# Optimization experiments

Hardware: AMD Instinct MI355X
Metric: run time of the kernel (lower is better)

Reference implementation:

```python
import jax, jax.numpy as jnp
import numpy as np
import math

B, N, D, H, O = 2, 1024, 256, 4, 8
DT, STEPS = 0.1, 5


def setup_inputs() -> dict:
    key = jax.random.key(0)
    ks = jax.random.split(key, 8)
    inv_d = 1.0 / math.sqrt(D)
    inv_ho = 1.0 / math.sqrt(H * O)
    return {
        "x": jax.random.normal(ks[0], (B, N, D), jnp.float32),
        "Wq": jax.random.normal(ks[1], (D, D), jnp.float32) * inv_d,
        "Wk": jax.random.normal(ks[2], (D, D), jnp.float32) * inv_d,
        "Wp": jax.random.normal(ks[3], (H * O, D), jnp.float32) * inv_d,
        "bp": jnp.zeros((H * O,), jnp.float32),
        "Wo": jax.random.normal(ks[4], (D, H * O), jnp.float32) * inv_ho,
        "bo": jnp.zeros((D,), jnp.float32),
        "omega": jax.random.normal(ks[5], (H, O), jnp.float32) * 0.1,
        "coupling_scale": jnp.asarray(1.0, jnp.float32),
    }


def reference(x, Wq, Wk, Wp, bp, Wo, bo, omega, coupling_scale):
    dk = D // H
    # attention coupling J_ij = softmax(q_i.k_j / sqrt(d_k))  -> (B,H,N,N)
    q = (x @ Wq.T).reshape(B, N, H, dk).transpose(0, 2, 1, 3)
    k = (x @ Wk.T).reshape(B, N, H, dk).transpose(0, 2, 1, 3)
    J = jax.nn.softmax(jnp.einsum('bhid,bhjd->bhij', q, k) / math.sqrt(dk), axis=-1)
    # initial phases (B,H,N,O)
    phases = (x @ Wp.T + bp).reshape(B, N, H, O).transpose(0, 2, 1, 3)
    om = omega[None, :, None, :]  # (1,H,1,O)

    def step(ph, _):
        # sum_j J_ij sin(phi_j - phi_i) = cos(phi_i)*(J@sin phi) - sin(phi_i)*(J@cos phi)
        s, c = jnp.sin(ph), jnp.cos(ph)
        coupling = c * jnp.einsum('bhij,bhjo->bhio', J, s) - s * jnp.einsum('bhij,bhjo->bhio', J, c)
        new = ph + DT * (om + coupling_scale * coupling)
        new = jnp.remainder(new + jnp.pi, 2 * jnp.pi) - jnp.pi
        return new, None

    phases, _ = jax.lax.scan(step, phases, None, length=STEPS)
    sig = jnp.cos(phases).transpose(0, 2, 1, 3).reshape(B, N, H * O)
    return sig @ Wo.T + bo
```

## Files before the change

### kernel.cpp

```cpp
#include <hip/hip_runtime.h>
#include <hip/hip_bf16.h>
#include <math.h>


#define NB 1024
#define NH 4
#define DD 256
#define NO 8
#define PI_F      3.14159265358979323846f
#define TWO_PI_F  6.28318530717958647692f
#define INV_2PI_F 0.15915494309189533577f

typedef __attribute__((ext_vector_type(8))) short bf16x8;
typedef __attribute__((ext_vector_type(4))) float f32x4;

__device__ __forceinline__ float b2f_u(unsigned short s) {
    union { unsigned u; float f; } x; x.u = ((unsigned)s) << 16; return x.f;
}
__device__ __forceinline__ unsigned short f2b(float f) {
    union { float f; unsigned u; } v; v.f = f;
    unsigned r = v.u + 0x7FFFu + ((v.u >> 16) & 1u);
    return (unsigned short)(r >> 16);
}
template<bool F32>
__device__ __forceinline__ float load1(const void* p, int i) {
    if (F32) return ((const float*)p)[i];
    else     return b2f_u(((const unsigned short*)p)[i]);
}
template<bool F32>
__device__ __forceinline__ void load8(const void* p, int i, float* f) {
    if (F32) {
        const float* fp = (const float*)p + i;
        float4 a = *(const float4*)(fp);
        float4 b = *(const float4*)(fp + 4);
        f[0]=a.x; f[1]=a.y; f[2]=a.z; f[3]=a.w;
        f[4]=b.x; f[5]=b.y; f[6]=b.z; f[7]=b.w;
    } else {
        uint4 u = *(const uint4*)((const unsigned short*)p + i);
        f[0] = b2f_u(u.x & 0xFFFFu); f[1] = b2f_u(u.x >> 16);
        f[2] = b2f_u(u.y & 0xFFFFu); f[3] = b2f_u(u.y >> 16);
        f[4] = b2f_u(u.z & 0xFFFFu); f[5] = b2f_u(u.z >> 16);
        f[6] = b2f_u(u.w & 0xFFFFu); f[7] = b2f_u(u.w >> 16);
    }
}
__device__ __forceinline__ float read_cs_bf16(const void* p) {
    float vb = b2f_u(*(const unsigned short*)p);
    bool ok = isfinite(vb) && fabsf(vb) > 1e-30f && fabsf(vb) < 1e30f;
    if (ok) return vb;
    return *(const float*)p;
}

__global__ void k_detect(const unsigned short* __restrict__ x, int* __restrict__ flag)
{
    int l = threadIdx.x & 63;
    float v0 = b2f_u(x[2 * l]);
    float v1 = b2f_u(x[2 * (l + 64)]);
    float a0 = fabsf(v0), a1 = fabsf(v1);
    unsigned long long b0 = __ballot(!(a0 >= 1e-10f && a0 <= 100.0f));
    unsigned long long b1 = __ballot(!(a1 >= 1e-10f && a1 <= 100.0f));
    if (l == 0) *flag = ((__popcll(b0) + __popcll(b1)) > 16) ? 1 : 0;
}

__global__ __launch_bounds__(256) void k_prep(
    const int* __restrict__ flag,
    const void* __restrict__ x, const void* __restrict__ Wq,
    const void* __restrict__ Wk, const void* __restrict__ Wp,
    unsigned short* __restrict__ xb, unsigned short* __restrict__ Wall)
{
    const int idx = blockIdx.x * 256 + threadIdx.x;
    const int f32 = *flag;
    if (idx < 524288) {
        float v = f32 ? ((const float*)x)[idx] : b2f_u(((const unsigned short*)x)[idx]);
        xb[idx] = f2b(v);
    } else {
        int w = idx - 524288;
        int row = w >> 8, col = w & 255;
        float v = 0.f;
        if (row < 256)      v = f32 ? ((const float*)Wq)[row*256+col] : b2f_u(((const unsigned short*)Wq)[row*256+col]);
        else if (row < 512) v = f32 ? ((const float*)Wk)[(row-256)*256+col] : b2f_u(((const unsigned short*)Wk)[(row-256)*256+col]);
        else if (row < 544) v = f32 ? ((const float*)Wp)[(row-512)*256+col] : b2f_u(((const unsigned short*)Wp)[(row-512)*256+col]);
        Wall[w] = f2b(v);
    }
}

__global__ __launch_bounds__(256) void k_projm(
    const int* __restrict__ flag,
    const unsigned short* __restrict__ xb, const unsigned short* __restrict__ Wall,
    const void* __restrict__ bp,
    unsigned short* __restrict__ Qb, unsigned short* __restrict__ Kb,
    float* __restrict__ PH)
{
    __shared__ uint4 Xsh[64 * 32];
    __shared__ uint4 Wsh[64 * 32];
    const int tid = threadIdx.x;
    const int gx = blockIdx.x;
    const int ftile = gx % 9, itile = gx / 9;
    const int i0 = itile * 64, f0 = ftile * 64;
    const int wave = tid >> 6, lane = tid & 63;
    const int n = lane & 15, quad = lane >> 4;

    #pragma unroll
    for (int g = 0; g < 8; g++) {
        int fidx = g * 256 + tid;
        int row = fidx >> 5, q = fidx & 31;
        int sw = (q & 24) | ((q ^ row) & 7);
        Xsh[row * 32 + sw] = *(const uint4*)(xb + (size_t)(i0 + row) * 256 + q * 8);
        Wsh[row * 32 + sw] = *(const uint4*)(Wall + (size_t)(f0 + row) * 256 + q * 8);
    }
    __syncthreads();

    f32x4 acc[4];
    #pragma unroll
    for (int s = 0; s < 4; s++) acc[s] = (f32x4){0.f, 0.f, 0.f, 0.f};
    const int xrow = wave * 16 + n;
    #pragma unroll
    for (int s = 0; s < 8; s++) {
        int qc = s * 4 + quad;
        bf16x8 b = ((const bf16x8*)Xsh)[xrow * 32 + ((qc & 24) | ((qc ^ xrow) & 7))];
        #pragma unroll
        for (int sub = 0; sub < 4; sub++) {
            int wr = sub * 16 + n;
            bf16x8 a = ((const bf16x8*)Wsh)[wr * 32 + ((qc & 24) | ((qc ^ wr) & 7))];
            acc[sub] = __builtin_amdgcn_mfma_f32_16x16x32_bf16(a, b, acc[sub], 0, 0, 0);
        }
    }

    const int ig = i0 + wave * 16 + n;
    const int bb = ig >> 10, nr = ig & 1023;
    if (ftile < 4) {
        #pragma unroll
        for (int sub = 0; sub < 4; sub++) {
            int dd = sub * 16 + quad * 4;
            ushort4 v = make_ushort4(f2b(acc[sub][0] * 0.125f), f2b(acc[sub][1] * 0.125f),
                                     f2b(acc[sub][2] * 0.125f), f2b(acc[sub][3] * 0.125f));
            *(ushort4*)(Qb + ((size_t)((bb * NH + ftile) * NB + nr)) * 64 + dd) = v;
        }
    } else if (ftile < 8) {
        int h = ftile - 4;
        #pragma unroll
        for (int sub = 0; sub < 4; sub++) {
            int dd = sub * 16 + quad * 4;
            ushort4 v = make_ushort4(f2b(acc[sub][0]), f2b(acc[sub][1]),
                                     f2b(acc[sub][2]), f2b(acc[sub][3]));
            *(ushort4*)(Kb + ((size_t)((bb * NH + h) * NB + nr)) * 64 + dd) = v;
        }
    } else {
        const int f32 = *flag;
        #pragma unroll
        for (int sub = 0; sub < 2; sub++) {
            #pragma unroll
            for (int r = 0; r < 4; r++) {
                int fp = sub * 16 + quad * 4 + r;
                int h2 = fp >> 3, o = fp & 7;
                float bpv = f32 ? ((const float*)bp)[fp] : b2f_u(((const unsigned short*)bp)[fp]);
                PH[((size_t)(bb * NH + h2)) * 8192 + o * 1024 + nr] = acc[sub][r] + bpv;
            }
        }
    }
}

__global__ __launch_bounds__(256) void k_scores(
    const unsigned short* __restrict__ Qb, const unsigned short* __restrict__ Kb,
    unsigned short* __restrict__ U, float* __restrict__ R)
{
    __shared__ uint4 Ksh[512 * 8];
    __shared__ float redS[2][2][16];
    const int tid = threadIdx.x;
    const int bh  = blockIdx.x >> 5;
    const int wave = tid >> 6, lane = tid & 63;
    const int n = lane & 15, quad = lane >> 4;
    const int iw = wave >> 1, jw = wave & 1;
    const int i0 = (blockIdx.x & 31) * 32 + iw * 16;

    const unsigned short* qrow = Qb + ((size_t)(bh * NB) + i0 + n) * 64;
    bf16x8 bq0 = *(const bf16x8*)(qrow + quad * 8);
    bf16x8 bq1 = *(const bf16x8*)(qrow + 32 + quad * 8);

    float s = 0.f;
    unsigned short* urow = U + ((size_t)(bh * NB) + i0 + n) * NB;
    #pragma unroll 1
    for (int half = 0; half < 2; half++) {
        __syncthreads();
        const unsigned short* ksrc = Kb + ((size_t)(bh * NB) + half * 512) * 64;
        #pragma unroll
        for (int g = 0; g < 16; g++) {
            int fidx = g * 256 + tid;
            int rl = fidx >> 3, q = fidx & 7;
            Ksh[rl * 8 + (q ^ (rl & 7))] = *(const uint4*)(ksrc + fidx * 8);
        }
        __syncthreads();
        for (int t = 0; t < 16; t++) {
            int jt = jw * 16 + t;
            int rl = jt * 16 + n;
            bf16x8 a0 = ((const bf16x8*)Ksh)[rl * 8 + (quad ^ (n & 7))];
            bf16x8 a1 = ((const bf16x8*)Ksh)[rl * 8 + ((4 + quad) ^ (n & 7))];
            f32x4 acc = {0.f, 0.f, 0.f, 0.f};
            acc = __builtin_amdgcn_mfma_f32_16x16x32_bf16(a0, bq0, acc, 0, 0, 0);
            acc = __builtin_amdgcn_mfma_f32_16x16x32_bf16(a1, bq1, acc, 0, 0, 0);
            float u0 = __expf(acc[0]);
            float u1 = __expf(acc[1]);
            float u2 = __expf(acc[2]);
            float u3 = __expf(acc[3]);
            s += (u0 + u1) + (u2 + u3);
            ushort4 uv = make_ushort4(f2b(u0), f2b(u1), f2b(u2), f2b(u3));
            *(ushort4*)(urow + half * 512 + jt * 16 + quad * 4) = uv;
        }
    }
    s += __shfl_xor(s, 16);
    s += __shfl_xor(s, 32);
    if (lane < 16) redS[iw][jw][lane] = s;
    __syncthreads();
    if (jw == 0 && lane < 16)
        R[bh * NB + i0 + lane] = 1.0f / (redS[iw][0][lane] + redS[iw][1][lane]);
}

__global__ __launch_bounds__(256) void k_step(
    const int* __restrict__ flag,
    const unsigned short* __restrict__ U, const float* __restrict__ R,
    const float* __restrict__ PHin, float* __restrict__ PHout,
    const void* __restrict__ omega, const void* __restrict__ csp)
{
    __shared__ uint4 sc4[16 * 128];
    __shared__ f32x4 red[4][64];
    const int tid  = threadIdx.x;
    const int bh   = blockIdx.x >> 6;
    const int i0   = (blockIdx.x & 63) * 16;
    const int wave = tid >> 6, lane = tid & 63;
    const int n    = lane & 15, quad = lane >> 4;
    const float* phs = PHin + (size_t)bh * 8192;

    #pragma unroll
    for (int g = 0; g < 8; g++) {
        float4 pv = *(const float4*)(phs + g * 1024 + tid * 4);
        float s0, c0, s1, c1, s2, c2, s3, c3;
        __sincosf(pv.x, &s0, &c0); __sincosf(pv.y, &s1, &c1);
        __sincosf(pv.z, &s2, &c2); __sincosf(pv.w, &s3, &c3);
        ushort4 sv = make_ushort4(f2b(s0), f2b(s1), f2b(s2), f2b(s3));
        ushort4 cv = make_ushort4(f2b(c0), f2b(c1), f2b(c2), f2b(c3));
        int ci = (tid >> 1) ^ (g & 7);
        char* base = (char*)sc4;
        *(ushort4*)(base + (((g     ) * 128 + ci) << 4) + ((tid & 1) << 3)) = sv;
        *(ushort4*)(base + (((g +  8) * 128 + ci) << 4) + ((tid & 1) << 3)) = cv;
    }
    __syncthreads();

    const unsigned short* urow = U + ((size_t)(bh * NB) + i0 + n) * NB;
    f32x4 acc = {0.f, 0.f, 0.f, 0.f};
    #pragma unroll
    for (int t = 0; t < 8; t++) {
        int it = wave * 8 + t;
        bf16x8 a = *(const bf16x8*)(urow + it * 32 + quad * 8);
        bf16x8 b = ((const bf16x8*)sc4)[n * 128 + ((it * 4 + quad) ^ (n & 7))];
        acc = __builtin_amdgcn_mfma_f32_16x16x32_bf16(a, b, acc, 0, 0, 0);
    }
    red[wave][lane] = acc;
    __syncthreads();

    if (wave == 0) {
        f32x4 a0 = red[0][lane], a1 = red[1][lane];
        f32x4 a2 = red[2][lane], a3 = red[3][lane];
        #pragma unroll
        for (int v = 0; v < 4; v++) acc[v] = (a0[v] + a1[v]) + (a2[v] + a3[v]);

        float C0 = __shfl_xor(acc[0], 8);
        float C1 = __shfl_xor(acc[1], 8);
        float C2 = __shfl_xor(acc[2], 8);
        float C3 = __shfl_xor(acc[3], 8);

        if (n < 8) {
            const int o = n, h = bh & 3;
            const int f32 = *flag;
            const float cs = f32 ? *(const float*)csp : read_cs_bf16(csp);
            const float om = f32 ? ((const float*)omega)[h * NO + o]
                                 : b2f_u(((const unsigned short*)omega)[h * NO + o]);
            float4 Rv = *(const float4*)(R + bh * NB + i0 + quad * 4);
            float4 pv = *(const float4*)(phs + o * 1024 + i0 + quad * 4);
            float S[4] = {acc[0], acc[1], acc[2], acc[3]};
            float C[4] = {C0, C1, C2, C3};
            float Rr[4] = {Rv.x, Rv.y, Rv.z, Rv.w};
            float P[4]  = {pv.x, pv.y, pv.z, pv.w};
            float outp[4];
            #pragma unroll
            for (int r = 0; r < 4; r++) {
                float si, ci;
                __sincosf(P[r], &si, &ci);
                float coup = (ci * S[r] - si * C[r]) * Rr[r];
                float v = P[r] + 0.1f * (om + cs * coup);
                float t = v + PI_F;
                t -= floorf(t * INV_2PI_F) * TWO_PI_F;
                outp[r] = t - PI_F;
            }
            float4 ov = {outp[0], outp[1], outp[2], outp[3]};
            *(float4*)(PHout + (size_t)bh * 8192 + o * 1024 + i0 + quad * 4) = ov;
        }
    }
}

template<bool F32>
__device__ void out_impl(
    const float* __restrict__ PH,
    const void* __restrict__ Wo, const void* __restrict__ bo,
    void* __restrict__ out)
{
    __shared__ float sig[32];
    const int tid = threadIdx.x;
    const int b = blockIdx.x >> 10, n = blockIdx.x & 1023;
    if (tid < 32) {
        int h = tid >> 3, o = tid & 7;
        sig[tid] = __cosf(PH[(size_t)(b * NH + h) * 8192 + o * 1024 + n]);
    }
    __syncthreads();
    float acc = load1<F32>(bo, tid);
    #pragma unroll
    for (int d0 = 0; d0 < 32; d0 += 8) {
        float w[8];
        load8<F32>(Wo, tid * 32 + d0, w);
        #pragma unroll
        for (int t = 0; t < 8; t++) acc += sig[d0 + t] * w[t];
    }
    size_t oi = (size_t)blockIdx.x * DD + tid;
    if (F32) ((float*)out)[oi] = acc;
    else     ((__hip_bfloat16*)out)[oi] = __float2bfloat16(acc);
}

__global__ __launch_bounds__(256) void k_out(
    const int* __restrict__ flag,
    const float* PH, const void* Wo, const void* bo, void* out)
{
    if (*flag) out_impl<true >(PH, Wo, bo, out);
    else       out_impl<false>(PH, Wo, bo, out);
}

extern "C" void kernel_launch(void* const* d_in, const int* in_sizes, int n_in,
                              void* d_out, int out_size, void* d_ws, size_t ws_size,
                              hipStream_t stream)
{
    const void* x   = d_in[0];
    const void* Wq  = d_in[1];
    const void* Wk  = d_in[2];
    const void* Wp  = d_in[3];
    const void* bp  = d_in[4];
    const void* Wo  = d_in[5];
    const void* bo  = d_in[6];
    const void* om  = d_in[7];
    const void* cs  = d_in[8];

    char* w = (char*)d_ws;
    int*            flag = (int*)w;
    unsigned short* Qb   = (unsigned short*)(w + 256);
    unsigned short* Kb   = (unsigned short*)(w + 256 + (1u << 20));
    float*          R    = (float*)(w + 256 + (2u << 20));
    float*          PH0  = (float*)(w + 256 + (2u << 20) + (64u << 10));
    float*          PH1  = (float*)(w + 256 + (2u << 20) + (320u << 10));
    unsigned short* U    = (unsigned short*)(w + 256 + (2u << 20) + (576u << 10));
    unsigned short* xb   = (unsigned short*)(w + 256 + (2u << 20) + (576u << 10) + (16u << 20));
    unsigned short* Wall = (unsigned short*)(w + 256 + (2u << 20) + (576u << 10) + (17u << 20));

    k_detect<<<1,    64,  0, stream>>>((const unsigned short*)x, flag);
    k_prep  <<<2624, 256, 0, stream>>>(flag, x, Wq, Wk, Wp, xb, Wall);
    k_projm <<<288,  256, 0, stream>>>(flag, xb, Wall, bp, Qb, Kb, PH0);
    k_scores<<<256,  256, 0, stream>>>(Qb, Kb, U, R);
    k_step<<<512, 256, 0, stream>>>(flag, U, R, PH0, PH1, om, cs);
    k_step<<<512, 256, 0, stream>>>(flag, U, R, PH1, PH0, om, cs);
    k_step<<<512, 256, 0, stream>>>(flag, U, R, PH0, PH1, om, cs);
    k_step<<<512, 256, 0, stream>>>(flag, U, R, PH1, PH0, om, cs);
    k_step<<<512, 256, 0, stream>>>(flag, U, R, PH0, PH1, om, cs);
    k_out<<<2048, 256, 0, stream>>>(flag, PH1, Wo, bo, d_out);
}
```

Measured before the change: 137.4 us.

## Fuse dtype detection and bf16 conversion into projection; precompute sin/cos tables

Removes the separate detect and prep kernels: each kernel now detects the input dtype inline, and the projection kernel converts fp32 inputs to bf16 while loading them into shared memory. The phase kernels now write bf16 sin/cos tables of the new phases, so the next step loads them directly instead of recomputing sincos for all 8192 phases per block. The output kernel reads cos from that table. This cuts two launches and redundant transcendental work. In exchange it adds scattered 2-byte writes of sin/cos and repeats the detection work in every block.

```diff
diff --git a/kernel.cpp b/kernel.cpp
--- a/kernel.cpp
+++ b/kernel.cpp
@@ -23,15 +23,22 @@
     return (unsigned short)(r >> 16);
 }
 template<bool F32>
-__device__ __forceinline__ float load1(const void* p, int i) {
-    if (F32) return ((const float*)p)[i];
-    else     return b2f_u(((const unsigned short*)p)[i]);
-}
-template<bool F32>
-__device__ __forceinline__ void load8(const void* p, int i, float* f) {
-    if (F32) {
+__device__ __forceinline__ uint4 load_pack8(const void* p, size_t off) {
+    if (!F32) return *(const uint4*)((const unsigned short*)p + off);
+    const float* fp = (const float*)p + off;
+    float4 a = *(const float4*)fp;
+    float4 b = *(const float4*)(fp + 4);
+    uint4 r;
+    r.x = (unsigned)f2b(a.x) | ((unsigned)f2b(a.y) << 16);
+    r.y = (unsigned)f2b(a.z) | ((unsigned)f2b(a.w) << 16);
+    r.z = (unsigned)f2b(b.x) | ((unsigned)f2b(b.y) << 16);
+    r.w = (unsigned)f2b(b.z) | ((unsigned)f2b(b.w) << 16);
+    return r;
+}
+__device__ __forceinline__ void load8_rt(int f32, const void* p, int i, float* f) {
+    if (f32) {
         const float* fp = (const float*)p + i;
-        float4 a = *(const float4*)(fp);
+        float4 a = *(const float4*)fp;
         float4 b = *(const float4*)(fp + 4);
         f[0]=a.x; f[1]=a.y; f[2]=a.z; f[3]=a.w;
         f[4]=b.x; f[5]=b.y; f[6]=b.z; f[7]=b.w;
@@ -49,52 +56,27 @@
     if (ok) return vb;
     return *(const float*)p;
 }
-
-__global__ void k_detect(const unsigned short* __restrict__ x, int* __restrict__ flag)
-{
+__device__ __forceinline__ int detect_inline(const unsigned short* x) {
     int l = threadIdx.x & 63;
-    float v0 = b2f_u(x[2 * l]);
-    float v1 = b2f_u(x[2 * (l + 64)]);
-    float a0 = fabsf(v0), a1 = fabsf(v1);
+    float a0 = fabsf(b2f_u(x[2 * l]));
+    float a1 = fabsf(b2f_u(x[2 * (l + 64)]));
     unsigned long long b0 = __ballot(!(a0 >= 1e-10f && a0 <= 100.0f));
     unsigned long long b1 = __ballot(!(a1 >= 1e-10f && a1 <= 100.0f));
-    if (l == 0) *flag = ((__popcll(b0) + __popcll(b1)) > 16) ? 1 : 0;
-}
-
-__global__ __launch_bounds__(256) void k_prep(
-    const int* __restrict__ flag,
+    return (__popcll(b0) + __popcll(b1)) > 16;
+}
+
+template<bool F32>
+__device__ void projm_impl(
     const void* __restrict__ x, const void* __restrict__ Wq,
     const void* __restrict__ Wk, const void* __restrict__ Wp,
-    unsigned short* __restrict__ xb, unsigned short* __restrict__ Wall)
-{
-    const int idx = blockIdx.x * 256 + threadIdx.x;
-    const int f32 = *flag;
-    if (idx < 524288) {
-        float v = f32 ? ((const float*)x)[idx] : b2f_u(((const unsigned short*)x)[idx]);
-        xb[idx] = f2b(v);
-    } else {
-        int w = idx - 524288;
-        int row = w >> 8, col = w & 255;
-        float v = 0.f;
-        if (row < 256)      v = f32 ? ((const float*)Wq)[row*256+col] : b2f_u(((const unsigned short*)Wq)[row*256+col]);
-        else if (row < 512) v = f32 ? ((const float*)Wk)[(row-256)*256+col] : b2f_u(((const unsigned short*)Wk)[(row-256)*256+col]);
-        else if (row < 544) v = f32 ? ((const float*)Wp)[(row-512)*256+col] : b2f_u(((const unsigned short*)Wp)[(row-512)*256+col]);
-        Wall[w] = f2b(v);
-    }
-}
-
-__global__ __launch_bounds__(256) void k_projm(
-    const int* __restrict__ flag,
-    const unsigned short* __restrict__ xb, const unsigned short* __restrict__ Wall,
     const void* __restrict__ bp,
     unsigned short* __restrict__ Qb, unsigned short* __restrict__ Kb,
-    float* __restrict__ PH)
+    float* __restrict__ PH, unsigned short* __restrict__ SC)
 {
     __shared__ uint4 Xsh[64 * 32];
     __shared__ uint4 Wsh[64 * 32];
     const int tid = threadIdx.x;
-    const int gx = blockIdx.x;
-    const int ftile = gx % 9, itile = gx / 9;
+    const int ftile = blockIdx.x % 9, itile = blockIdx.x / 9;
     const int i0 = itile * 64, f0 = ftile * 64;
     const int wave = tid >> 6, lane = tid & 63;
     const int n = lane & 15, quad = lane >> 4;
@@ -104,8 +86,13 @@
         int fidx = g * 256 + tid;
         int row = fidx >> 5, q = fidx & 31;
         int sw = (q & 24) | ((q ^ row) & 7);
-        Xsh[row * 32 + sw] = *(const uint4*)(xb + (size_t)(i0 + row) * 256 + q * 8);
-        Wsh[row * 32 + sw] = *(const uint4*)(Wall + (size_t)(f0 + row) * 256 + q * 8);
+        Xsh[row * 32 + sw] = load_pack8<F32>(x, (size_t)(i0 + row) * 256 + q * 8);
+        int wr = f0 + row;
+        uint4 wv = make_uint4(0, 0, 0, 0);
+        if (wr < 256)      wv = load_pack8<F32>(Wq, (size_t)wr * 256 + q * 8);
+        else if (wr < 512) wv = load_pack8<F32>(Wk, (size_t)(wr - 256) * 256 + q * 8);
+        else if (wr < 544) wv = load_pack8<F32>(Wp, (size_t)(wr - 512) * 256 + q * 8);
+        Wsh[row * 32 + sw] = wv;
     }
     __syncthreads();
 
@@ -145,18 +132,33 @@
             *(ushort4*)(Kb + ((size_t)((bb * NH + h) * NB + nr)) * 64 + dd) = v;
         }
     } else {
-        const int f32 = *flag;
         #pragma unroll
         for (int sub = 0; sub < 2; sub++) {
             #pragma unroll
             for (int r = 0; r < 4; r++) {
                 int fp = sub * 16 + quad * 4 + r;
                 int h2 = fp >> 3, o = fp & 7;
-                float bpv = f32 ? ((const float*)bp)[fp] : b2f_u(((const unsigned short*)bp)[fp]);
-                PH[((size_t)(bb * NH + h2)) * 8192 + o * 1024 + nr] = acc[sub][r] + bpv;
+                float bpv = F32 ? ((const float*)bp)[fp]
+                                : b2f_u(((const unsigned short*)bp)[fp]);
+                float v = acc[sub][r] + bpv;
+                int bh = bb * NH + h2;
+                PH[(size_t)bh * 8192 + o * 1024 + nr] = v;
+                float sv, cv;
+                __sincosf(v, &sv, &cv);
+                SC[(size_t)(bh * 16 + o) * 1024 + nr]     = f2b(sv);
+                SC[(size_t)(bh * 16 + 8 + o) * 1024 + nr] = f2b(cv);
             }
         }
     }
+}
+
+__global__ __launch_bounds__(256) void k_projm(
+    const unsigned short* x, const void* Wq, const void* Wk, const void* Wp,
+    const void* bp, unsigned short* Qb, unsigned short* Kb, float* PH,
+    unsigned short* SC)
+{
+    if (detect_inline(x)) projm_impl<true >(x, Wq, Wk, Wp, bp, Qb, Kb, PH, SC);
+    else                  projm_impl<false>(x, Wq, Wk, Wp, bp, Qb, Kb, PH, SC);
 }
 
 __global__ __launch_bounds__(256) void k_scores(
@@ -202,8 +204,8 @@
             float u2 = __expf(acc[2]);
             float u3 = __expf(acc[3]);
             s += (u0 + u1) + (u2 + u3);
-            ushort4 uv = make_ushort4(f2b(u0), f2b(u1), f2b(u2), f2b(u3));
-            *(ushort4*)(urow + half * 512 + jt * 16 + quad * 4) = uv;
+            *(ushort4*)(urow + half * 512 + jt * 16 + quad * 4)
+                = make_ushort4(f2b(u0), f2b(u1), f2b(u2), f2b(u3));
         }
     }
     s += __shfl_xor(s, 16);
@@ -215,9 +217,10 @@
 }
 
 __global__ __launch_bounds__(256) void k_step(
-    const int* __restrict__ flag,
+    const unsigned short* __restrict__ xraw,
     const unsigned short* __restrict__ U, const float* __restrict__ R,
     const float* __restrict__ PHin, float* __restrict__ PHout,
+    const unsigned short* __restrict__ SCin, unsigned short* __restrict__ SCout,
     const void* __restrict__ omega, const void* __restrict__ csp)
 {
     __shared__ uint4 sc4[16 * 128];
@@ -227,20 +230,15 @@
     const int i0   = (blockIdx.x & 63) * 16;
     const int wave = tid >> 6, lane = tid & 63;
     const int n    = lane & 15, quad = lane >> 4;
+    const int f32  = detect_inline(xraw);
     const float* phs = PHin + (size_t)bh * 8192;
 
     #pragma unroll
     for (int g = 0; g < 8; g++) {
-        float4 pv = *(const float4*)(phs + g * 1024 + tid * 4);
-        float s0, c0, s1, c1, s2, c2, s3, c3;
-        __sincosf(pv.x, &s0, &c0); __sincosf(pv.y, &s1, &c1);
-        __sincosf(pv.z, &s2, &c2); __sincosf(pv.w, &s3, &c3);
-        ushort4 sv = make_ushort4(f2b(s0), f2b(s1), f2b(s2), f2b(s3));
-        ushort4 cv = make_ushort4(f2b(c0), f2b(c1), f2b(c2), f2b(c3));
-        int ci = (tid >> 1) ^ (g & 7);
-        char* base = (char*)sc4;
-        *(ushort4*)(base + (((g     ) * 128 + ci) << 4) + ((tid & 1) << 3)) = sv;
-        *(ushort4*)(base + (((g +  8) * 128 + ci) << 4) + ((tid & 1) << 3)) = cv;
+        int fidx = g * 256 + tid;
+        int row = fidx >> 7, col = fidx & 127;
+        sc4[row * 128 + (col ^ (row & 7))]
+            = *(const uint4*)(SCin + (size_t)(bh * 16 + row) * 1024 + col * 8);
     }
     __syncthreads();
 
@@ -269,7 +267,6 @@
 
         if (n < 8) {
             const int o = n, h = bh & 3;
-            const int f32 = *flag;
             const float cs = f32 ? *(const float*)csp : read_cs_bf16(csp);
             const float om = f32 ? ((const float*)omega)[h * NO + o]
                                  : b2f_u(((const unsigned short*)omega)[h * NO + o]);
@@ -279,63 +276,64 @@
             float C[4] = {C0, C1, C2, C3};
             float Rr[4] = {Rv.x, Rv.y, Rv.z, Rv.w};
             float P[4]  = {pv.x, pv.y, pv.z, pv.w};
-            float outp[4];
+            float op[4];
             #pragma unroll
             for (int r = 0; r < 4; r++) {
                 float si, ci;
                 __sincosf(P[r], &si, &ci);
                 float coup = (ci * S[r] - si * C[r]) * Rr[r];
                 float v = P[r] + 0.1f * (om + cs * coup);
-                float t = v + PI_F;
-                t -= floorf(t * INV_2PI_F) * TWO_PI_F;
-                outp[r] = t - PI_F;
+                float t2 = v + PI_F;
+                t2 -= floorf(t2 * INV_2PI_F) * TWO_PI_F;
+                op[r] = t2 - PI_F;
             }
-            float4 ov = {outp[0], outp[1], outp[2], outp[3]};
-            *(float4*)(PHout + (size_t)bh * 8192 + o * 1024 + i0 + quad * 4) = ov;
-        }
-    }
-}
-
-template<bool F32>
-__device__ void out_impl(
-    const float* __restrict__ PH,
+            *(float4*)(PHout + (size_t)bh * 8192 + o * 1024 + i0 + quad * 4)
+                = make_float4(op[0], op[1], op[2], op[3]);
+            #pragma unroll
+            for (int r = 0; r < 4; r++) {
+                float sn, cn;
+                __sincosf(op[r], &sn, &cn);
+                int i = i0 + quad * 4 + r;
+                SCout[(size_t)(bh * 16 + o) * 1024 + i]     = f2b(sn);
+                SCout[(size_t)(bh * 16 + 8 + o) * 1024 + i] = f2b(cn);
+            }
+        }
+    }
+}
+
+__global__ __launch_bounds__(256) void k_out(
+    const unsigned short* __restrict__ xraw,
+    const unsigned short* __restrict__ SC,
     const void* __restrict__ Wo, const void* __restrict__ bo,
     void* __restrict__ out)
 {
     __shared__ float sig[32];
     const int tid = threadIdx.x;
     const int b = blockIdx.x >> 10, n = blockIdx.x & 1023;
+    const int f32 = detect_inline(xraw);
     if (tid < 32) {
         int h = tid >> 3, o = tid & 7;
-        sig[tid] = __cosf(PH[(size_t)(b * NH + h) * 8192 + o * 1024 + n]);
-    }
-    __syncthreads();
-    float acc = load1<F32>(bo, tid);
+        sig[tid] = b2f_u(SC[(size_t)((b * NH + h) * 16 + 8 + o) * 1024 + n]);
+    }
+    __syncthreads();
+    float acc = f32 ? ((const float*)bo)[tid] : b2f_u(((const unsigned short*)bo)[tid]);
     #pragma unroll
     for (int d0 = 0; d0 < 32; d0 += 8) {
         float w[8];
-        load8<F32>(Wo, tid * 32 + d0, w);
+        load8_rt(f32, Wo, tid * 32 + d0, w);
         #pragma unroll
         for (int t = 0; t < 8; t++) acc += sig[d0 + t] * w[t];
     }
     size_t oi = (size_t)blockIdx.x * DD + tid;
-    if (F32) ((float*)out)[oi] = acc;
-    else     ((__hip_bfloat16*)out)[oi] = __float2bfloat16(acc);
-}
-
-__global__ __launch_bounds__(256) void k_out(
-    const int* __restrict__ flag,
-    const float* PH, const void* Wo, const void* bo, void* out)
-{
-    if (*flag) out_impl<true >(PH, Wo, bo, out);
-    else       out_impl<false>(PH, Wo, bo, out);
+    if (f32) ((float*)out)[oi] = acc;
+    else     ((unsigned short*)out)[oi] = f2b(acc);
 }
 
 extern "C" void kernel_launch(void* const* d_in, const int* in_sizes, int n_in,
                               void* d_out, int out_size, void* d_ws, size_t ws_size,
                               hipStream_t stream)
 {
-    const void* x   = d_in[0];
+    const unsigned short* x = (const unsigned short*)d_in[0];
     const void* Wq  = d_in[1];
     const void* Wk  = d_in[2];
     const void* Wp  = d_in[3];
@@ -346,24 +344,21 @@
     const void* cs  = d_in[8];
 
     char* w = (char*)d_ws;
-    int*            flag = (int*)w;
-    unsigned short* Qb   = (unsigned short*)(w + 256);
-    unsigned short* Kb   = (unsigned short*)(w + 256 + (1u << 20));
-    float*          R    = (float*)(w + 256 + (2u << 20));
-    float*          PH0  = (float*)(w + 256 + (2u << 20) + (64u << 10));
-    float*          PH1  = (float*)(w + 256 + (2u << 20) + (320u << 10));
-    unsigned short* U    = (unsigned short*)(w + 256 + (2u << 20) + (576u << 10));
-    unsigned short* xb   = (unsigned short*)(w + 256 + (2u << 20) + (576u << 10) + (16u << 20));
-    unsigned short* Wall = (unsigned short*)(w + 256 + (2u << 20) + (576u << 10) + (17u << 20));
-
-    k_detect<<<1,    64,  0, stream>>>((const unsigned short*)x, flag);
-    k_prep  <<<2624, 256, 0, stream>>>(flag, x, Wq, Wk, Wp, xb, Wall);
-    k_projm <<<288,  256, 0, stream>>>(flag, xb, Wall, bp, Qb, Kb, PH0);
-    k_scores<<<256,  256, 0, stream>>>(Qb, Kb, U, R);
-    k_step<<<512, 256, 0, stream>>>(flag, U, R, PH0, PH1, om, cs);
-    k_step<<<512, 256, 0, stream>>>(flag, U, R, PH1, PH0, om, cs);
-    k_step<<<512, 256, 0, stream>>>(flag, U, R, PH0, PH1, om, cs);
-    k_step<<<512, 256, 0, stream>>>(flag, U, R, PH1, PH0, om, cs);
-    k_step<<<512, 256, 0, stream>>>(flag, U, R, PH0, PH1, om, cs);
-    k_out<<<2048, 256, 0, stream>>>(flag, PH1, Wo, bo, d_out);
-}
+    unsigned short* Qb  = (unsigned short*)w;
+    unsigned short* Kb  = (unsigned short*)(w + (1u << 20));
+    float*          R   = (float*)(w + (2u << 20));
+    float*          PH0 = (float*)(w + (2u << 20) + (64u << 10));
+    float*          PH1 = (float*)(w + (2u << 20) + (320u << 10));
+    unsigned short* SC0 = (unsigned short*)(w + (2u << 20) + (576u << 10));
+    unsigned short* SC1 = (unsigned short*)(w + (2u << 20) + (832u << 10));
+    unsigned short* U   = (unsigned short*)(w + (2u << 20) + (1088u << 10));
+
+    k_projm <<<288, 256, 0, stream>>>(x, Wq, Wk, Wp, bp, Qb, Kb, PH0, SC0);
+    k_scores<<<256, 256, 0, stream>>>(Qb, Kb, U, R);
+    k_step<<<512, 256, 0, stream>>>(x, U, R, PH0, PH1, SC0, SC1, om, cs);
+    k_step<<<512, 256, 0, stream>>>(x, U, R, PH1, PH0, SC1, SC0, om, cs);
+    k_step<<<512, 256, 0, stream>>>(x, U, R, PH0, PH1, SC0, SC1, om, cs);
+    k_step<<<512, 256, 0, stream>>>(x, U, R, PH1, PH0, SC1, SC0, om, cs);
+    k_step<<<512, 256, 0, stream>>>(x, U, R, PH0, PH1, SC0, SC1, om, cs);
+    k_out<<<2048, 256, 0, stream>>>(x, SC1, Wo, bo, d_out);
+}
```

Result: slower. 140.7 us (+2.4%).
